# Kernel tuning notes

Hardware: AMD Instinct MI355X
Metric: run time of the kernel (lower is better)

Reference implementation:

```python
import jax, jax.numpy as jnp
import numpy as np

N_NODES = 50000
N_EDGES = 1600000
D_IN = 512
D_OUT = 512


def setup_inputs() -> dict:
    key = jax.random.key(0)
    ks = jax.random.split(key, 10)
    x = jax.random.normal(ks[0], (N_NODES, D_IN), dtype=jnp.float32)
    w0 = jax.random.normal(ks[1], (D_IN, D_OUT), dtype=jnp.float32) * 0.02
    w1 = jax.random.normal(ks[2], (D_IN, D_OUT), dtype=jnp.float32) * 0.02
    b = jax.random.normal(ks[3], (D_OUT,), dtype=jnp.float32) * 0.02
    vals0 = jax.random.uniform(ks[4], (N_EDGES,), dtype=jnp.float32)
    vals1 = jax.random.uniform(ks[5], (N_EDGES,), dtype=jnp.float32)
    rows0 = jax.random.randint(ks[6], (N_EDGES,), 0, N_NODES, dtype=jnp.int32)
    cols0 = jax.random.randint(ks[7], (N_EDGES,), 0, N_NODES, dtype=jnp.int32)
    rows1 = jax.random.randint(ks[8], (N_EDGES,), 0, N_NODES, dtype=jnp.int32)
    cols1 = jax.random.randint(ks[9], (N_EDGES,), 0, N_NODES, dtype=jnp.int32)
    return {"x": x, "w0": w0, "w1": w1, "b": b,
            "vals0": vals0, "vals1": vals1,
            "rows0": rows0, "cols0": cols0, "rows1": rows1, "cols1": cols1}


def _spmm(rows, cols, vals, dense):
    # sparse [N,N] @ dense [N,D]: gather source rows, scale, scatter-add to dest rows
    gathered = vals[:, None] * dense[cols]  # [E, D]
    return jax.ops.segment_sum(gathered, rows, num_segments=N_NODES)


def reference(x, w0, w1, b, vals0, vals1, rows0, cols0, rows1, cols1):
    # dropout rate is 0.0 (dropout=False), so input passes through unchanged
    pre0 = x @ w0  # [N, D_out]
    pre1 = x @ w1
    s0 = _spmm(rows0, cols0, vals0, pre0)
    s1 = _spmm(rows1, cols1, vals1, pre1)
    out = s0 + s1 + b  # add_n over supports, then bias
    return jax.nn.relu(out)
```

## Files before the change

kernel.cpp:

```cpp
#include <hip/hip_runtime.h>
#include <cstdint>
#include <cstddef>

#define N_NODES 50000
#define N_EDGES 1600000
#define D 512
#define MPAD 50048
#define NPX 6250
#define CAP 80
#define TILE_SHIFT 11
#define NTILES 25

typedef __attribute__((ext_vector_type(8))) short bf16x8;
typedef __attribute__((ext_vector_type(4))) float f32x4;
typedef __attribute__((ext_vector_type(8))) unsigned short u16x8;
typedef __attribute__((ext_vector_type(4))) int i32x4;

static __device__ __forceinline__ unsigned short f2bf(float f) {
  unsigned u = __float_as_uint(f);
  u += 0x7fffu + ((u >> 16) & 1u);
  return (unsigned short)(u >> 16);
}

__global__ __launch_bounds__(256) void prep(const float* __restrict__ x,
                                            const float* __restrict__ w0,
                                            const float* __restrict__ w1,
                                            unsigned char* __restrict__ xq,
                                            float* __restrict__ scale,
                                            unsigned short* __restrict__ wbT,
                                            int* __restrict__ cnt) {
  __shared__ float ts[64][68];
  const int t = threadIdx.x;
  if (blockIdx.x < 12500) {
    const int lane = t & 63;
    const int wave = t >> 6;
    const int n = blockIdx.x * 4 + wave;
    const float* xr = x + (size_t)n * D + lane * 8;
    f32x4 f0 = __builtin_nontemporal_load((const f32x4*)xr);
    f32x4 f1 = __builtin_nontemporal_load((const f32x4*)xr + 1);
    float m = fmaxf(fmaxf(fmaxf(fabsf(f0[0]), fabsf(f0[1])), fmaxf(fabsf(f0[2]), fabsf(f0[3]))),
                    fmaxf(fmaxf(fabsf(f1[0]), fabsf(f1[1])), fmaxf(fabsf(f1[2]), fabsf(f1[3]))));
    #pragma unroll
    for (int off = 32; off >= 1; off >>= 1) m = fmaxf(m, __shfl_xor(m, off, 64));
    m = fmaxf(m, 1e-20f);
    const float inv = 127.0f / m;
    int q[8];
    q[0] = (int)rintf(f0[0] * inv) + 128; q[1] = (int)rintf(f0[1] * inv) + 128;
    q[2] = (int)rintf(f0[2] * inv) + 128; q[3] = (int)rintf(f0[3] * inv) + 128;
    q[4] = (int)rintf(f1[0] * inv) + 128; q[5] = (int)rintf(f1[1] * inv) + 128;
    q[6] = (int)rintf(f1[2] * inv) + 128; q[7] = (int)rintf(f1[3] * inv) + 128;
    unsigned lo = (q[0] & 0xff) | ((q[1] & 0xff) << 8) | ((q[2] & 0xff) << 16) | ((unsigned)(q[3] & 0xff) << 24);
    unsigned hi = (q[4] & 0xff) | ((q[5] & 0xff) << 8) | ((q[6] & 0xff) << 16) | ((unsigned)(q[7] & 0xff) << 24);
    *(uint2*)(xq + (size_t)n * D + lane * 8) = make_uint2(lo, hi);
    if (lane == 0) scale[n] = m * (1.0f / 127.0f);
  } else if (blockIdx.x < 12628) {
    const int bid2 = blockIdx.x - 12500;
    const int m = bid2 >> 6;
    const int tile = bid2 & 63;
    const int k0 = (tile >> 3) * 64;
    const int j0 = (tile & 7) * 64;
    const float* W = m ? w1 : w0;
    const int tr = t >> 4;
    const int tc = (t & 15) * 4;
    #pragma unroll
    for (int it = 0; it < 4; ++it) {
      int kk = tr + it * 16;
      float4 v = *(const float4*)&W[(size_t)(k0 + kk) * 512 + j0 + tc];
      ts[kk][tc] = v.x; ts[kk][tc + 1] = v.y; ts[kk][tc + 2] = v.z; ts[kk][tc + 3] = v.w;
    }
    __syncthreads();
    const int jl = t >> 3;
    const int kl = (t & 7) * 8;
    #pragma unroll
    for (int it = 0; it < 2; ++it) {
      int j = jl + it * 32;
      u16x8 o;
      #pragma unroll
      for (int q2 = 0; q2 < 8; ++q2) o[q2] = f2bf(ts[kl + q2][j]);
      *(u16x8*)&wbT[(size_t)(j0 + j) * 1024 + m * 512 + k0 + kl] = o;
    }
  } else {
    int q2 = (int)(blockIdx.x - 12628) * 256 + t;
    if (q2 < 25000) ((i32x4*)cnt)[q2] = (i32x4)0;
  }
}

__global__ __launch_bounds__(256) void fill_bucket(
    const int* __restrict__ r0, const int* __restrict__ co0, const float* __restrict__ v0,
    const int* __restrict__ r1, const int* __restrict__ co1, const float* __restrict__ v1,
    const float* __restrict__ scale,
    int* __restrict__ cnt0, int* __restrict__ cnt1,
    unsigned* __restrict__ e0, unsigned* __restrict__ e1) {
  const int nq = N_EDGES / 4;
  const int lo = (int)(blockIdx.x & 7) * NPX;
  const int hi = lo + NPX;
  const int stride = (1024 >> 3) * 256;
  for (int i = (int)(blockIdx.x >> 3) * 256 + threadIdx.x; i < 2 * nq; i += stride) {
    if (i < nq) {
      i32x4 r = ((const i32x4*)r0)[i];
      i32x4 c = ((const i32x4*)co0)[i];
      f32x4 v = ((const f32x4*)v0)[i];
      #pragma unroll
      for (int k = 0; k < 4; ++k) {
        if (r[k] >= lo && r[k] < hi) {
          int slot = atomicAdd(&cnt0[r[k]], 1);
          if (slot < CAP)
            e0[(size_t)r[k] * CAP + slot] =
                (unsigned)c[k] | ((unsigned)f2bf(v[k] * scale[c[k]]) << 16);
        }
      }
    } else {
      int j = i - nq;
      i32x4 r = ((const i32x4*)r1)[j];
      i32x4 c = ((const i32x4*)co1)[j];
      f32x4 v = ((const f32x4*)v1)[j];
      #pragma unroll
      for (int k = 0; k < 4; ++k) {
        if (r[k] >= lo && r[k] < hi) {
          int slot = atomicAdd(&cnt1[r[k]], 1);
          if (slot < CAP)
            e1[(size_t)r[k] * CAP + slot] =
                (unsigned)c[k] | ((unsigned)f2bf(v[k] * scale[c[k]]) << 16);
        }
      }
    }
  }
}

static __device__ __forceinline__ void acc8u(float* a, uint2 q, float v) {
  a[0] += v * (float)(q.x & 0xffu);
  a[1] += v * (float)((q.x >> 8) & 0xffu);
  a[2] += v * (float)((q.x >> 16) & 0xffu);
  a[3] += v * (float)((q.x >> 24) & 0xffu);
  a[4] += v * (float)(q.y & 0xffu);
  a[5] += v * (float)((q.y >> 8) & 0xffu);
  a[6] += v * (float)((q.y >> 16) & 0xffu);
  a[7] += v * (float)((q.y >> 24) & 0xffu);
}

__global__ __launch_bounds__(256) void spmm_sorted(const unsigned char* __restrict__ xq,
    const int* __restrict__ cnt0, const unsigned* __restrict__ e0,
    const int* __restrict__ cnt1, const unsigned* __restrict__ e1,
    unsigned short* __restrict__ s) {
  __shared__ unsigned sed[4][2][CAP];
  __shared__ int cur[4][2][NTILES];
  __shared__ unsigned short starts[4][2][NTILES + 1];
  const int t = threadIdx.x;
  const int lane = t & 63;
  const int wave = t >> 6;
  const int n = blockIdx.x * 4 + wave;
  const int c0 = lane * 8;

  int deg0 = cnt0[n]; if (deg0 > CAP) deg0 = CAP;
  int deg1 = cnt1[n]; if (deg1 > CAP) deg1 = CAP;
  const unsigned* eb0 = e0 + (size_t)n * CAP;
  const unsigned* eb1 = e1 + (size_t)n * CAP;

  for (int b = lane; b < 2 * NTILES; b += 64) ((int*)cur[wave])[b] = 0;
  __syncthreads();

  unsigned my0[2] = {0u, 0u}, my1[2] = {0u, 0u};
  #pragma unroll
  for (int q = 0; q < 2; ++q) {
    int p = lane + q * 64;
    if (p < deg0) {
      unsigned m = eb0[p]; my0[q] = m;
      atomicAdd(&cur[wave][0][(m & 0xffffu) >> TILE_SHIFT], 1);
    }
    if (p < deg1) {
      unsigned m = eb1[p]; my1[q] = m;
      atomicAdd(&cur[wave][1][(m & 0xffffu) >> TILE_SHIFT], 1);
    }
  }
  __syncthreads();

  if (lane < 2) {
    int acc2 = 0;
    for (int t2 = 0; t2 < NTILES; ++t2) {
      starts[wave][lane][t2] = (unsigned short)acc2;
      int h = cur[wave][lane][t2];
      cur[wave][lane][t2] = acc2;
      acc2 += h;
    }
    starts[wave][lane][NTILES] = (unsigned short)acc2;
  }
  __syncthreads();

  #pragma unroll
  for (int q = 0; q < 2; ++q) {
    int p = lane + q * 64;
    if (p < deg0) {
      unsigned m = my0[q];
      int pos = atomicAdd(&cur[wave][0][(m & 0xffffu) >> TILE_SHIFT], 1);
      sed[wave][0][pos] = m;
    }
    if (p < deg1) {
      unsigned m = my1[q];
      int pos = atomicAdd(&cur[wave][1][(m & 0xffffu) >> TILE_SHIFT], 1);
      sed[wave][1][pos] = m;
    }
  }
  __syncthreads();

  float acc[2][8] = {};
  float sumv[2] = {0.f, 0.f};
  for (int t2 = 0; t2 < NTILES; ++t2) {
    #pragma unroll
    for (int sup = 0; sup < 2; ++sup) {
      float* a = acc[sup];
      float sv = 0.f;
      int p = starts[wave][sup][t2];
      const int pe = starts[wave][sup][t2 + 1];
      for (; p + 1 < pe; p += 2) {
        unsigned mA = sed[wave][sup][p];
        unsigned mB = sed[wave][sup][p + 1];
        uint2 qA = *(const uint2*)(xq + (size_t)(mA & 0xffffu) * D + c0);
        uint2 qB = *(const uint2*)(xq + (size_t)(mB & 0xffffu) * D + c0);
        float vA = __uint_as_float(mA & 0xffff0000u);
        float vB = __uint_as_float(mB & 0xffff0000u);
        acc8u(a, qA, vA);
        acc8u(a, qB, vB);
        sv += vA + vB;
      }
      if (p < pe) {
        unsigned m = sed[wave][sup][p];
        uint2 q = *(const uint2*)(xq + (size_t)(m & 0xffffu) * D + c0);
        float v = __uint_as_float(m & 0xffff0000u);
        acc8u(a, q, v);
        sv += v;
      }
      sumv[sup] += sv;
    }
  }

  u16x8 o0, o1;
  #pragma unroll
  for (int i = 0; i < 8; ++i) {
    o0[i] = f2bf(acc[0][i] - 128.0f * sumv[0]);
    o1[i] = f2bf(acc[1][i] - 128.0f * sumv[1]);
  }
  *(u16x8*)(s + (size_t)n * 1024 + c0) = o0;
  *(u16x8*)(s + (size_t)n * 1024 + 512 + c0) = o1;
}

#define BM 128
#define BN 256
#define BK 32

__global__ __launch_bounds__(256) void gemm_out(const unsigned short* __restrict__ s,
                                                const unsigned short* __restrict__ wbT,
                                                const float* __restrict__ bias,
                                                float* __restrict__ out) {
  __shared__ __align__(16) unsigned short As[2][BM * BK];
  __shared__ __align__(16) unsigned short Bs[2][BN * BK];
  const int t = threadIdx.x;
  const int lane = t & 63;
  const int wave = t >> 6;
  const int wm = wave >> 1, wn = wave & 1;
  const int lr = lane & 15;
  const int slot = lane >> 4;
  const int m0 = blockIdx.y * BM;
  const int n0 = blockIdx.x * BN;

  f32x4 acc[4][8] = {};
  const int NT = 1024 / BK;

  auto STAGE = [&](int buf, int kt) {
    #pragma unroll
    for (int i = 0; i < 2; ++i) {
      int ch = i * 256 + t;
      int row = ch >> 2;
      int sl = ch & 3;
      int ke = (sl ^ ((row >> 1) & 3)) * 8;
      const unsigned short* ga = s + (size_t)(m0 + row) * 1024 + kt * BK + ke;
      __builtin_amdgcn_global_load_lds(
          (const __attribute__((address_space(1))) unsigned int*)ga,
          (__attribute__((address_space(3))) unsigned int*)(&As[buf][ch * 8]), 16, 0, 0);
    }
    #pragma unroll
    for (int i = 0; i < 4; ++i) {
      int ch = i * 256 + t;
      int row = ch >> 2;
      int sl = ch & 3;
      int ke = (sl ^ ((row >> 1) & 3)) * 8;
      const unsigned short* gb = wbT + (size_t)(n0 + row) * 1024 + kt * BK + ke;
      __builtin_amdgcn_global_load_lds(
          (const __attribute__((address_space(1))) unsigned int*)gb,
          (__attribute__((address_space(3))) unsigned int*)(&Bs[buf][ch * 8]), 16, 0, 0);
    }
  };

  STAGE(0, 0);
  __syncthreads();

  for (int kt = 0; kt < NT; ++kt) {
    const int cur = kt & 1;
    if (kt + 1 < NT) STAGE(cur ^ 1, kt + 1);

    bf16x8 a[4], b[8];
    #pragma unroll
    for (int i = 0; i < 4; ++i) {
      int row = wm * 64 + i * 16 + lr;
      a[i] = *(const bf16x8*)&As[cur][row * BK + (slot ^ ((row >> 1) & 3)) * 8];
    }
    #pragma unroll
    for (int j = 0; j < 8; ++j) {
      int row = wn * 128 + j * 16 + lr;
      b[j] = *(const bf16x8*)&Bs[cur][row * BK + (slot ^ ((row >> 1) & 3)) * 8];
    }
    #pragma unroll
    for (int i = 0; i < 4; ++i)
      #pragma unroll
      for (int j = 0; j < 8; ++j)
        acc[i][j] = __builtin_amdgcn_mfma_f32_16x16x32_bf16(a[i], b[j], acc[i][j], 0, 0, 0);
    __syncthreads();
  }

  float bj[8];
  #pragma unroll
  for (int j = 0; j < 8; ++j) bj[j] = bias[n0 + wn * 128 + j * 16 + lr];

  const int orow = slot * 4;
  #pragma unroll
  for (int i = 0; i < 4; ++i) {
    #pragma unroll
    for (int j = 0; j < 8; ++j) {
      #pragma unroll
      for (int r = 0; r < 4; ++r) {
        int row = m0 + wm * 64 + i * 16 + orow + r;
        if (row < N_NODES) {
          int col = n0 + wn * 128 + j * 16 + lr;
          __builtin_nontemporal_store(fmaxf(acc[i][j][r] + bj[j], 0.f),
                                      out + (size_t)row * 512 + col);
        }
      }
    }
  }
}

extern "C" void kernel_launch(void* const* d_in, const int* in_sizes, int n_in,
                              void* d_out, int out_size, void* d_ws, size_t ws_size,
                              hipStream_t stream) {
  const float* x     = (const float*)d_in[0];
  const float* w0    = (const float*)d_in[1];
  const float* w1    = (const float*)d_in[2];
  const float* bias  = (const float*)d_in[3];
  const float* vals0 = (const float*)d_in[4];
  const float* vals1 = (const float*)d_in[5];
  const int*   rows0 = (const int*)d_in[6];
  const int*   cols0 = (const int*)d_in[7];
  const int*   rows1 = (const int*)d_in[8];
  const int*   cols1 = (const int*)d_in[9];
  float* out = (float*)d_out;

  char* ws = (char*)d_ws;
  size_t off = 0;
  auto alloc = [&](size_t bytes) -> char* {
    char* p = ws + off;
    off += (bytes + 255) & ~(size_t)255;
    return p;
  };
  unsigned char*  xq    = (unsigned char*)alloc((size_t)N_NODES * D);
  float*          scale = (float*)alloc((size_t)N_NODES * sizeof(float));
  unsigned short* wbT   = (unsigned short*)alloc((size_t)512 * 1024 * 2);
  unsigned short* s     = (unsigned short*)alloc((size_t)MPAD * 1024 * 2);
  int* cnt  = (int*)alloc(2 * N_NODES * sizeof(int));
  unsigned* e0 = (unsigned*)alloc((size_t)N_NODES * CAP * 4);
  unsigned* e1 = (unsigned*)alloc((size_t)N_NODES * CAP * 4);

  prep<<<12726, 256, 0, stream>>>(x, w0, w1, xq, scale, wbT, cnt);
  fill_bucket<<<1024, 256, 0, stream>>>(rows0, cols0, vals0, rows1, cols1, vals1,
                                        scale, cnt, cnt + N_NODES, e0, e1);
  spmm_sorted<<<N_NODES / 4, 256, 0, stream>>>(xq, cnt, e0, cnt + N_NODES, e1, s);
  gemm_out<<<dim3(512 / BN, MPAD / BM), 256, 0, stream>>>(s, wbT, bias, out);
}
```

Measured before the change: 499.7 us.

## Quantize aggregated features and weights to int8 and use i8 MFMA GEMM

```diff
diff --git a/kernel.cpp b/kernel.cpp
--- a/kernel.cpp
+++ b/kernel.cpp
@@ -27,9 +27,12 @@
                                             const float* __restrict__ w1,
                                             unsigned char* __restrict__ xq,
                                             float* __restrict__ scale,
-                                            unsigned short* __restrict__ wbT,
+                                            signed char* __restrict__ wbT,
+                                            float* __restrict__ wscale,
                                             int* __restrict__ cnt) {
   __shared__ float ts[64][68];
+  __shared__ float cmax[4][64];
+  __shared__ float cinv[64];
   const int t = threadIdx.x;
   if (blockIdx.x < 12500) {
     const int lane = t & 63;
@@ -60,6 +63,23 @@
     const int k0 = (tile >> 3) * 64;
     const int j0 = (tile & 7) * 64;
     const float* W = m ? w1 : w0;
+    const int lane = t & 63;
+    const int wv = t >> 6;
+    float mx = 0.f;
+    #pragma unroll 8
+    for (int k = wv * 256; k < wv * 256 + 256; ++k) {
+      const float* Wk = (k < 512) ? (w0 + (size_t)k * 512) : (w1 + (size_t)(k - 512) * 512);
+      mx = fmaxf(mx, fabsf(Wk[j0 + lane]));
+    }
+    cmax[wv][lane] = mx;
+    __syncthreads();
+    if (t < 64) {
+      float c = fmaxf(fmaxf(cmax[0][t], cmax[1][t]), fmaxf(cmax[2][t], cmax[3][t]));
+      c = fmaxf(c, 1e-20f);
+      cinv[t] = 127.0f / c;
+      if (m == 0 && k0 == 0) wscale[j0 + t] = c * (1.0f / 127.0f);
+    }
+    __syncthreads();
     const int tr = t >> 4;
     const int tc = (t & 15) * 4;
     #pragma unroll
@@ -74,10 +94,19 @@
     #pragma unroll
     for (int it = 0; it < 2; ++it) {
       int j = jl + it * 32;
-      u16x8 o;
-      #pragma unroll
-      for (int q2 = 0; q2 < 8; ++q2) o[q2] = f2bf(ts[kl + q2][j]);
-      *(u16x8*)&wbT[(size_t)(j0 + j) * 1024 + m * 512 + k0 + kl] = o;
+      float inv = cinv[j];
+      unsigned lo = 0, hi = 0;
+      #pragma unroll
+      for (int q2 = 0; q2 < 4; ++q2) {
+        int q = (int)rintf(ts[kl + q2][j] * inv);
+        lo |= ((unsigned)(q & 0xff)) << (8 * q2);
+      }
+      #pragma unroll
+      for (int q2 = 4; q2 < 8; ++q2) {
+        int q = (int)rintf(ts[kl + q2][j] * inv);
+        hi |= ((unsigned)(q & 0xff)) << (8 * (q2 - 4));
+      }
+      *(uint2*)&wbT[(size_t)(j0 + j) * 1024 + m * 512 + k0 + kl] = make_uint2(lo, hi);
     }
   } else {
     int q2 = (int)(blockIdx.x - 12628) * 256 + t;
@@ -141,7 +170,7 @@
 __global__ __launch_bounds__(256) void spmm_sorted(const unsigned char* __restrict__ xq,
     const int* __restrict__ cnt0, const unsigned* __restrict__ e0,
     const int* __restrict__ cnt1, const unsigned* __restrict__ e1,
-    unsigned short* __restrict__ s) {
+    signed char* __restrict__ sq, float* __restrict__ sscale) {
   __shared__ unsigned sed[4][2][CAP];
   __shared__ int cur[4][2][NTILES];
   __shared__ unsigned short starts[4][2][NTILES + 1];
@@ -233,26 +262,44 @@
     }
   }
 
-  u16x8 o0, o1;
+  float f0[8], f1[8];
   #pragma unroll
   for (int i = 0; i < 8; ++i) {
-    o0[i] = f2bf(acc[0][i] - 128.0f * sumv[0]);
-    o1[i] = f2bf(acc[1][i] - 128.0f * sumv[1]);
-  }
-  *(u16x8*)(s + (size_t)n * 1024 + c0) = o0;
-  *(u16x8*)(s + (size_t)n * 1024 + 512 + c0) = o1;
+    f0[i] = acc[0][i] - 128.0f * sumv[0];
+    f1[i] = acc[1][i] - 128.0f * sumv[1];
+  }
+  float m = 0.f;
+  #pragma unroll
+  for (int i = 0; i < 8; ++i) m = fmaxf(m, fmaxf(fabsf(f0[i]), fabsf(f1[i])));
+  #pragma unroll
+  for (int off = 32; off >= 1; off >>= 1) m = fmaxf(m, __shfl_xor(m, off, 64));
+  m = fmaxf(m, 1e-20f);
+  const float inv = 127.0f / m;
+  unsigned lo0 = 0, hi0 = 0, lo1 = 0, hi1 = 0;
+  #pragma unroll
+  for (int i = 0; i < 4; ++i) {
+    int q0 = (int)rintf(f0[i] * inv);     lo0 |= ((unsigned)(q0 & 0xff)) << (8 * i);
+    int q4 = (int)rintf(f0[i + 4] * inv); hi0 |= ((unsigned)(q4 & 0xff)) << (8 * i);
+    int r0 = (int)rintf(f1[i] * inv);     lo1 |= ((unsigned)(r0 & 0xff)) << (8 * i);
+    int r4 = (int)rintf(f1[i + 4] * inv); hi1 |= ((unsigned)(r4 & 0xff)) << (8 * i);
+  }
+  *(uint2*)(sq + (size_t)n * 1024 + c0) = make_uint2(lo0, hi0);
+  *(uint2*)(sq + (size_t)n * 1024 + 512 + c0) = make_uint2(lo1, hi1);
+  if (lane == 0) sscale[n] = m * (1.0f / 127.0f);
 }
 
 #define BM 128
 #define BN 256
-#define BK 32
-
-__global__ __launch_bounds__(256) void gemm_out(const unsigned short* __restrict__ s,
-                                                const unsigned short* __restrict__ wbT,
+#define BKB 64
+
+__global__ __launch_bounds__(256) void gemm_out(const signed char* __restrict__ sq,
+                                                const signed char* __restrict__ wbT,
+                                                const float* __restrict__ sscale,
+                                                const float* __restrict__ wscale,
                                                 const float* __restrict__ bias,
                                                 float* __restrict__ out) {
-  __shared__ __align__(16) unsigned short As[2][BM * BK];
-  __shared__ __align__(16) unsigned short Bs[2][BN * BK];
+  __shared__ __align__(16) signed char As[2][BM * BKB];
+  __shared__ __align__(16) signed char Bs[2][BN * BKB];
   const int t = threadIdx.x;
   const int lane = t & 63;
   const int wave = t >> 6;
@@ -262,8 +309,8 @@
   const int m0 = blockIdx.y * BM;
   const int n0 = blockIdx.x * BN;
 
-  f32x4 acc[4][8] = {};
-  const int NT = 1024 / BK;
+  i32x4 acc[4][8] = {};
+  const int NT = 1024 / BKB;
 
   auto STAGE = [&](int buf, int kt) {
     #pragma unroll
@@ -271,22 +318,22 @@
       int ch = i * 256 + t;
       int row = ch >> 2;
       int sl = ch & 3;
-      int ke = (sl ^ ((row >> 1) & 3)) * 8;
-      const unsigned short* ga = s + (size_t)(m0 + row) * 1024 + kt * BK + ke;
+      int keb = (sl ^ ((row >> 1) & 3)) * 16;
+      const signed char* ga = sq + (size_t)(m0 + row) * 1024 + kt * BKB + keb;
       __builtin_amdgcn_global_load_lds(
           (const __attribute__((address_space(1))) unsigned int*)ga,
-          (__attribute__((address_space(3))) unsigned int*)(&As[buf][ch * 8]), 16, 0, 0);
+          (__attribute__((address_space(3))) unsigned int*)(&As[buf][ch * 16]), 16, 0, 0);
     }
     #pragma unroll
     for (int i = 0; i < 4; ++i) {
       int ch = i * 256 + t;
       int row = ch >> 2;
       int sl = ch & 3;
-      int ke = (sl ^ ((row >> 1) & 3)) * 8;
-      const unsigned short* gb = wbT + (size_t)(n0 + row) * 1024 + kt * BK + ke;
+      int keb = (sl ^ ((row >> 1) & 3)) * 16;
+      const signed char* gb = wbT + (size_t)(n0 + row) * 1024 + kt * BKB + keb;
       __builtin_amdgcn_global_load_lds(
           (const __attribute__((address_space(1))) unsigned int*)gb,
-          (__attribute__((address_space(3))) unsigned int*)(&Bs[buf][ch * 8]), 16, 0, 0);
+          (__attribute__((address_space(3))) unsigned int*)(&Bs[buf][ch * 16]), 16, 0, 0);
     }
   };
 
@@ -297,30 +344,42 @@
     const int cur = kt & 1;
     if (kt + 1 < NT) STAGE(cur ^ 1, kt + 1);
 
-    bf16x8 a[4], b[8];
+    i32x4 a[4], b[8];
     #pragma unroll
     for (int i = 0; i < 4; ++i) {
       int row = wm * 64 + i * 16 + lr;
-      a[i] = *(const bf16x8*)&As[cur][row * BK + (slot ^ ((row >> 1) & 3)) * 8];
+      a[i] = *(const i32x4*)&As[cur][row * BKB + (slot ^ ((row >> 1) & 3)) * 16];
     }
     #pragma unroll
     for (int j = 0; j < 8; ++j) {
       int row = wn * 128 + j * 16 + lr;
-      b[j] = *(const bf16x8*)&Bs[cur][row * BK + (slot ^ ((row >> 1) & 3)) * 8];
+      b[j] = *(const i32x4*)&Bs[cur][row * BKB + (slot ^ ((row >> 1) & 3)) * 16];
     }
     #pragma unroll
     for (int i = 0; i < 4; ++i)
       #pragma unroll
       for (int j = 0; j < 8; ++j)
-        acc[i][j] = __builtin_amdgcn_mfma_f32_16x16x32_bf16(a[i], b[j], acc[i][j], 0, 0, 0);
+        acc[i][j] = __builtin_amdgcn_mfma_i32_16x16x64_i8(a[i], b[j], acc[i][j], 0, 0, 0);
     __syncthreads();
   }
 
-  float bj[8];
-  #pragma unroll
-  for (int j = 0; j < 8; ++j) bj[j] = bias[n0 + wn * 128 + j * 16 + lr];
-
+  float bj[8], ws_[8];
+  #pragma unroll
+  for (int j = 0; j < 8; ++j) {
+    int col = n0 + wn * 128 + j * 16 + lr;
+    bj[j] = bias[col];
+    ws_[j] = wscale[col];
+  }
   const int orow = slot * 4;
+  float ss[4][4];
+  #pragma unroll
+  for (int i = 0; i < 4; ++i)
+    #pragma unroll
+    for (int r = 0; r < 4; ++r) {
+      int row = m0 + wm * 64 + i * 16 + orow + r;
+      ss[i][r] = (row < N_NODES) ? sscale[row] : 0.f;
+    }
+
   #pragma unroll
   for (int i = 0; i < 4; ++i) {
     #pragma unroll
@@ -330,8 +389,8 @@
         int row = m0 + wm * 64 + i * 16 + orow + r;
         if (row < N_NODES) {
           int col = n0 + wn * 128 + j * 16 + lr;
-          __builtin_nontemporal_store(fmaxf(acc[i][j][r] + bj[j], 0.f),
-                                      out + (size_t)row * 512 + col);
+          float v = (float)acc[i][j][r] * ss[i][r] * ws_[j] + bj[j];
+          __builtin_nontemporal_store(fmaxf(v, 0.f), out + (size_t)row * 512 + col);
         }
       }
     }
@@ -360,17 +419,19 @@
     off += (bytes + 255) & ~(size_t)255;
     return p;
   };
-  unsigned char*  xq    = (unsigned char*)alloc((size_t)N_NODES * D);
-  float*          scale = (float*)alloc((size_t)N_NODES * sizeof(float));
-  unsigned short* wbT   = (unsigned short*)alloc((size_t)512 * 1024 * 2);
-  unsigned short* s     = (unsigned short*)alloc((size_t)MPAD * 1024 * 2);
+  unsigned char*  xq     = (unsigned char*)alloc((size_t)N_NODES * D);
+  float*          scale  = (float*)alloc((size_t)N_NODES * sizeof(float));
+  signed char*    wbT    = (signed char*)alloc((size_t)512 * 1024);
+  float*          wscale = (float*)alloc(512 * sizeof(float));
+  signed char*    sq     = (signed char*)alloc((size_t)MPAD * 1024);
+  float*          sscale = (float*)alloc((size_t)MPAD * sizeof(float));
   int* cnt  = (int*)alloc(2 * N_NODES * sizeof(int));
   unsigned* e0 = (unsigned*)alloc((size_t)N_NODES * CAP * 4);
   unsigned* e1 = (unsigned*)alloc((size_t)N_NODES * CAP * 4);
 
-  prep<<<12726, 256, 0, stream>>>(x, w0, w1, xq, scale, wbT, cnt);
+  prep<<<12726, 256, 0, stream>>>(x, w0, w1, xq, scale, wbT, wscale, cnt);
   fill_bucket<<<1024, 256, 0, stream>>>(rows0, cols0, vals0, rows1, cols1, vals1,
                                         scale, cnt, cnt + N_NODES, e0, e1);
-  spmm_sorted<<<N_NODES / 4, 256, 0, stream>>>(xq, cnt, e0, cnt + N_NODES, e1, s);
-  gemm_out<<<dim3(512 / BN, MPAD / BM), 256, 0, stream>>>(s, wbT, bias, out);
-}
+  spmm_sorted<<<N_NODES / 4, 256, 0, stream>>>(xq, cnt, e0, cnt + N_NODES, e1, sq, sscale);
+  gemm_out<<<dim3(512 / BN, MPAD / BM), 256, 0, stream>>>(sq, wbT, sscale, wscale, bias, out);
+}
```

Result: no change. 509.5 us (+2.0%).
